# Optimization experiments

Measured on AMD Instinct MI355X. Metric: run time of the kernel, lower is better.

Reference implementation:

```python
import jax, jax.numpy as jnp
import numpy as np
import math

BATCH, SEQ, D_MODEL, HEADS = 2, 2048, 1024, 16
DK = D_MODEL // HEADS  # 64
THETA = 10000.0


def _init_linear(key, d_in, d_out):
    std = math.sqrt(2.0 / (d_in + d_out))
    return (jax.random.truncated_normal(key, -3.0, 3.0, (d_in, d_out), jnp.float32) * std)


def setup_inputs() -> dict:
    key = jax.random.key(0)
    kx, kq, kk, kv, ko = jax.random.split(key, 5)
    x = jax.random.normal(kx, (BATCH, SEQ, D_MODEL), jnp.float32)
    W_Q = _init_linear(kq, D_MODEL, D_MODEL)
    W_K = _init_linear(kk, D_MODEL, D_MODEL)
    W_V = _init_linear(kv, D_MODEL, D_MODEL)
    W_O = _init_linear(ko, D_MODEL, D_MODEL)
    token_positions = jnp.arange(SEQ, dtype=jnp.int64 if jax.config.jax_enable_x64 else jnp.int32)
    # RoPE tables: angle[i, k] = i / theta**(2k/d_k), shape [max_seq_len, d_k//2]
    pos = jnp.arange(SEQ, dtype=jnp.float32)[:, None]
    inv_freq = THETA ** (-2.0 * jnp.arange(DK // 2, dtype=jnp.float32) / DK)
    angles = pos * inv_freq
    return {
        "x": x,
        "token_positions": token_positions,
        "W_Q": W_Q,
        "W_K": W_K,
        "W_V": W_V,
        "W_O": W_O,
        "cos": jnp.cos(angles),
        "sin": jnp.sin(angles),
    }


def _apply_rope(t, cos_p, sin_p):
    # t: [B, H, S, DK]; cos_p/sin_p: [S, DK//2] (already gathered by position)
    t_even = t[..., 0::2]
    t_odd = t[..., 1::2]
    even_rot = cos_p * t_even - sin_p * t_odd
    odd_rot = sin_p * t_even + cos_p * t_odd
    # interleave back: [..., DK//2, 2] -> [..., DK]
    return jnp.stack([even_rot, odd_rot], axis=-1).reshape(t.shape)


def reference(x, token_positions, W_Q, W_K, W_V, W_O, cos, sin):
    B, S, D = x.shape
    H, dk = HEADS, D // HEADS
    # QKV projections, split into heads: [B, S, D] -> [B, H, S, dk]
    def proj(W):
        return jnp.einsum("bsd,de->bse", x, W).reshape(B, S, H, dk).transpose(0, 2, 1, 3)
    Q, K, V = proj(W_Q), proj(W_K), proj(W_V)
    cos_p = cos[token_positions]  # [S, dk//2]
    sin_p = sin[token_positions]
    Q = _apply_rope(Q, cos_p, sin_p)
    K = _apply_rope(K, cos_p, sin_p)
    scores = jnp.einsum("bhqd,bhkd->bhqk", Q, K) / jnp.sqrt(jnp.asarray(dk, x.dtype))
    causal = jnp.tril(jnp.ones((S, S), dtype=bool))
    scores = jnp.where(causal, scores, -jnp.inf)
    attn = jax.nn.softmax(scores, axis=-1)
    out = jnp.einsum("bhqk,bhkd->bhqd", attn, V)  # [B, H, S, dk]
    out = out.transpose(0, 2, 1, 3).reshape(B, S, D)
    return jnp.einsum("bsd,de->bse", out, W_O)
```

## Files before the change

### kernel.cpp

```cpp
#include <hip/hip_runtime.h>

typedef unsigned short u16;
typedef unsigned int   u32;
typedef __bf16  bf16x8 __attribute__((ext_vector_type(8)));
typedef float   f32x4  __attribute__((ext_vector_type(4)));
typedef u32     u32x4  __attribute__((ext_vector_type(4)));

#define SEQ    2048
#define HEADS  16
#define DM     1024
#define NBH    32
#define NBS    4096

#define LOG2E  1.4426950408889634f

__device__ __forceinline__ u16 f2b(float f) {
    u32 x;
    __builtin_memcpy(&x, &f, 4);
    return (u16)((x + 0x7fffu + ((x >> 16) & 1u)) >> 16);
}

__device__ __forceinline__ u32 pkc(float lo, float hi) {
    __bf16 a = (__bf16)lo, b = (__bf16)hi;
    u16 x, y;
    __builtin_memcpy(&x, &a, 2);
    __builtin_memcpy(&y, &b, 2);
    return (u32)x | ((u32)y << 16);
}

__device__ __forceinline__ bf16x8 ld_bf8(const u16* p) {
    return *(const bf16x8*)p;
}

__device__ __forceinline__ void gl_lds16(const u16* g, __bf16* l) {
    __builtin_amdgcn_global_load_lds(
        (__attribute__((address_space(1))) void*)g,
        (__attribute__((address_space(3))) void*)l,
        16, 0, 0);
}

__global__ __launch_bounds__(256) void transpose_wqkv(const float* __restrict__ Wq,
                                                      const float* __restrict__ Wk,
                                                      const float* __restrict__ Wv,
                                                      u16* __restrict__ WqkvT) {
    __shared__ u16 tile[64][65];
    const int z  = blockIdx.z;
    const float* src = (z == 0) ? Wq : (z == 1) ? Wk : Wv;
    const int k0 = blockIdx.x * 64, n0 = blockIdx.y * 64;
    const int tid = threadIdx.x;
    for (int i = 0; i < 16; ++i) {
        int e = i * 256 + tid;
        int r = e >> 6, c = e & 63;
        tile[r][c] = f2b(src[(size_t)(k0 + r) * DM + n0 + c]);
    }
    __syncthreads();
    u16* dst = WqkvT + (size_t)z * DM * DM;
    for (int i = 0; i < 16; ++i) {
        int e = i * 256 + tid;
        int r = e >> 6, c = e & 63;
        dst[(size_t)(n0 + r) * DM + k0 + c] = tile[c][r];
    }
}

__global__ __launch_bounds__(256) void transpose_wo(const float* __restrict__ Wo,
                                                    u16* __restrict__ WoT) {
    __shared__ u16 tile[64][65];
    const int k0 = blockIdx.x * 64, n0 = blockIdx.y * 64;
    const int tid = threadIdx.x;
    for (int i = 0; i < 16; ++i) {
        int e = i * 256 + tid;
        int r = e >> 6, c = e & 63;
        tile[r][c] = f2b(Wo[(size_t)(k0 + r) * DM + n0 + c]);
    }
    __syncthreads();
    for (int i = 0; i < 16; ++i) {
        int e = i * 256 + tid;
        int r = e >> 6, c = e & 63;
        WoT[(size_t)(n0 + r) * DM + k0 + c] = tile[c][r];
    }
}

__global__ __launch_bounds__(256) void cvt_x(const float* __restrict__ x,
                                             u16* __restrict__ xb) {
    int t = blockIdx.x * 256 + threadIdx.x;
    const float* p = x + (size_t)t * 8;
    f32x4 a = *(const f32x4*)p;
    f32x4 b = *(const f32x4*)(p + 4);
    u32x4 v;
    v[0] = pkc(a[0], a[1]);
    v[1] = pkc(a[2], a[3]);
    v[2] = pkc(b[0], b[1]);
    v[3] = pkc(b[2], b[3]);
    *(u32x4*)(xb + (size_t)t * 8) = v;
}

__global__ __launch_bounds__(256) void gemm_qkv(const u16* __restrict__ Ab,
                                                const u16* __restrict__ Bt,
                                                u16* __restrict__ Qp,
                                                u16* __restrict__ Kp,
                                                u16* __restrict__ Vt) {
    __shared__ __attribute__((aligned(16))) __bf16 As[128 * 64];
    __shared__ __attribute__((aligned(16))) __bf16 Bs[128 * 64];
    const int tid  = threadIdx.x;
    const int wave = tid >> 6, lane = tid & 63;
    const int quad = lane >> 4, col = lane & 15;
    const int wm = wave >> 1, wn = wave & 1;
    const int m0 = blockIdx.x * 128, n0 = blockIdx.y * 128;
    const int srow = tid >> 3;
    const int aslot = (((tid & 7) ^ (srow & 7)) << 3);
    const int c7 = col & 7;

    f32x4 zero = {0.f, 0.f, 0.f, 0.f};
    f32x4 acc[4][4];
    for (int i = 0; i < 4; ++i)
        for (int j = 0; j < 4; ++j) acc[i][j] = zero;

    for (int k0 = 0; k0 < DM; k0 += 64) {
        __syncthreads();
#pragma unroll
        for (int p = 0; p < 4; ++p)
            gl_lds16(Ab + (size_t)(m0 + p * 32 + srow) * DM + k0 + aslot,
                     &As[p * 2048 + tid * 8]);
#pragma unroll
        for (int p = 0; p < 4; ++p)
            gl_lds16(Bt + (size_t)(n0 + p * 32 + srow) * DM + k0 + aslot,
                     &Bs[p * 2048 + tid * 8]);
        __syncthreads();
#pragma unroll
        for (int ks = 0; ks < 2; ++ks) {
            const int rsl = ((((ks << 2) | quad) ^ c7) << 3);
            bf16x8 af[4], bfr[4];
#pragma unroll
            for (int mt = 0; mt < 4; ++mt)
                af[mt] = *(const bf16x8*)&As[(wm * 64 + mt * 16 + col) * 64 + rsl];
#pragma unroll
            for (int nt = 0; nt < 4; ++nt)
                bfr[nt] = *(const bf16x8*)&Bs[(wn * 64 + nt * 16 + col) * 64 + rsl];
#pragma unroll
            for (int mt = 0; mt < 4; ++mt)
#pragma unroll
                for (int nt = 0; nt < 4; ++nt)
                    acc[mt][nt] = __builtin_amdgcn_mfma_f32_16x16x32_bf16(
                        af[mt], bfr[nt], acc[mt][nt], 0, 0, 0);
        }
    }

    for (int mt = 0; mt < 4; ++mt)
        for (int nt = 0; nt < 4; ++nt) {
            int cc = n0 + wn * 64 + nt * 16 + col;
            int which = cc >> 10;
            int c1 = cc & 1023;
            int h = c1 >> 6, d = c1 & 63;
            for (int r = 0; r < 4; ++r) {
                int row = m0 + wm * 64 + mt * 16 + quad * 4 + r;
                int b = row >> 11, s = row & (SEQ - 1);
                u16 val = f2b(acc[mt][nt][r]);
                size_t bh = (size_t)(b * HEADS + h);
                if (which == 0)
                    Qp[(bh * SEQ + s) * 64 + d] = val;
                else if (which == 1)
                    Kp[(bh * SEQ + s) * 64 + d] = val;
                else
                    Vt[(bh * 64 + d) * SEQ + s] = val;
            }
        }
}

__global__ __launch_bounds__(256) void gemm_wo(const u16* __restrict__ A,
                                               const u16* __restrict__ Bt,
                                               float* __restrict__ C) {
    __shared__ __attribute__((aligned(16))) __bf16 As[128 * 64];
    __shared__ __attribute__((aligned(16))) __bf16 Bs[64 * 64];
    const int tid  = threadIdx.x;
    const int wave = tid >> 6, lane = tid & 63;
    const int quad = lane >> 4, col = lane & 15;
    const int m0 = blockIdx.x * 128, n0 = blockIdx.y * 64;
    const int srow = tid >> 3;
    const int aslot = (((tid & 7) ^ (srow & 7)) << 3);
    const int c7 = col & 7;

    f32x4 zero = {0.f, 0.f, 0.f, 0.f};
    f32x4 acc[2][4];
    for (int i = 0; i < 2; ++i)
        for (int j = 0; j < 4; ++j) acc[i][j] = zero;

    for (int k0 = 0; k0 < DM; k0 += 64) {
        __syncthreads();
#pragma unroll
        for (int p = 0; p < 4; ++p)
            gl_lds16(A + (size_t)(m0 + p * 32 + srow) * DM + k0 + aslot,
                     &As[p * 2048 + tid * 8]);
#pragma unroll
        for (int p = 0; p < 2; ++p)
            gl_lds16(Bt + (size_t)(n0 + p * 32 + srow) * DM + k0 + aslot,
                     &Bs[p * 2048 + tid * 8]);
        __syncthreads();
#pragma unroll
        for (int ks = 0; ks < 2; ++ks) {
            const int rsl = ((((ks << 2) | quad) ^ c7) << 3);
            bf16x8 af[2], bfr[4];
#pragma unroll
            for (int mt = 0; mt < 2; ++mt)
                af[mt] = *(const bf16x8*)&As[(wave * 32 + mt * 16 + col) * 64 + rsl];
#pragma unroll
            for (int nt = 0; nt < 4; ++nt)
                bfr[nt] = *(const bf16x8*)&Bs[(nt * 16 + col) * 64 + rsl];
#pragma unroll
            for (int mt = 0; mt < 2; ++mt)
#pragma unroll
                for (int nt = 0; nt < 4; ++nt)
                    acc[mt][nt] = __builtin_amdgcn_mfma_f32_16x16x32_bf16(
                        af[mt], bfr[nt], acc[mt][nt], 0, 0, 0);
        }
    }

    for (int mt = 0; mt < 2; ++mt)
        for (int nt = 0; nt < 4; ++nt)
            for (int r = 0; r < 4; ++r) {
                int row = m0 + wave * 32 + mt * 16 + quad * 4 + r;
                int cc  = n0 + nt * 16 + col;
                C[(size_t)row * DM + cc] = acc[mt][nt][r];
            }
}

__global__ __launch_bounds__(256) void rope_qk(u16* __restrict__ Qp,
                                               u16* __restrict__ Kp,
                                               const float* __restrict__ cosT,
                                               const float* __restrict__ sinT) {
    int t = blockIdx.x * 256 + threadIdx.x;
    int g  = t & 7;
    int s  = (t >> 3) & (SEQ - 1);
    int hh = (t >> 14) & (HEADS - 1);
    int b  = t >> 18;

    f32x4 cv = *(const f32x4*)&cosT[s * 32 + g * 4];
    f32x4 sv = *(const f32x4*)&sinT[s * 32 + g * 4];

    const float QS = 0.125f * LOG2E;
    size_t addr = (((size_t)(b * HEADS + hh)) * SEQ + s) * 64 + g * 8;
    u32x4 q4 = *(const u32x4*)(Qp + addr);
    u32x4 k4 = *(const u32x4*)(Kp + addr);
    u32x4 qo4, ko4;
#pragma unroll
    for (int j = 0; j < 4; ++j) {
        u32 q2 = q4[j], k2 = k4[j];
        u32 qe_b = (q2 & 0xffff) << 16, qo_b = q2 & 0xffff0000u;
        u32 ke_b = (k2 & 0xffff) << 16, ko_b = k2 & 0xffff0000u;
        float qe, qo, ke, ko;
        __builtin_memcpy(&qe, &qe_b, 4); __builtin_memcpy(&qo, &qo_b, 4);
        __builtin_memcpy(&ke, &ke_b, 4); __builtin_memcpy(&ko, &ko_b, 4);
        qo4[j] = (u32)f2b(QS * (cv[j] * qe - sv[j] * qo)) |
                 ((u32)f2b(QS * (sv[j] * qe + cv[j] * qo)) << 16);
        ko4[j] = (u32)f2b(cv[j] * ke - sv[j] * ko) |
                 ((u32)f2b(sv[j] * ke + cv[j] * ko) << 16);
    }
    *(u32x4*)(Qp + addr) = qo4;
    *(u32x4*)(Kp + addr) = ko4;
}

__global__ __launch_bounds__(256, 3) void flash_attn(const u16* __restrict__ Qp,
                                                     const u16* __restrict__ Kp,
                                                     const u16* __restrict__ Vt,
                                                     u16* __restrict__ O) {
    __shared__ float os[4][32][68];
    __shared__ float mM[4][32];
    __shared__ float mL[4][32];
    const int tid  = threadIdx.x;
    const int wave = tid >> 6, lane = tid & 63;
    const int quad = lane >> 4, col = lane & 15;
    const bool hi5 = lane >= 32;
    const bool hi4 = (lane & 16) != 0;
    const int bh = blockIdx.x;
    const int b = bh >> 4, h = bh & 15;
    const int qt = 63 - blockIdx.y;
    const int q0 = qt * 32;

    const u16* Qb = Qp + (size_t)bh * SEQ * 64;
    const u16* Kb = Kp + (size_t)bh * SEQ * 64;
    const u16* Vb = Vt + (size_t)bh * 64 * SEQ;

    bf16x8 bq00 = ld_bf8(Qb + (size_t)(q0 + col) * 64 + quad * 8);
    bf16x8 bq01 = ld_bf8(Qb + (size_t)(q0 + col) * 64 + 32 + quad * 8);
    bf16x8 bq10 = ld_bf8(Qb + (size_t)(q0 + 16 + col) * 64 + quad * 8);
    bf16x8 bq11 = ld_bf8(Qb + (size_t)(q0 + 16 + col) * 64 + 32 + quad * 8);

    f32x4 zero = {0.f, 0.f, 0.f, 0.f};
    f32x4 o0[4] = {zero, zero, zero, zero};
    f32x4 o1[4] = {zero, zero, zero, zero};
    float m0_ = -1e30f, m1_ = -1e30f;
    float lp0 = 0.f, lp1 = 0.f;

    const int nkt = qt + 1;
    int kt = wave;
    bf16x8 ck00, ck01, ck10, ck11, cv0, cv1, cv2, cv3;
    if (kt < nkt) {
        const int kb = kt << 5;
        ck00 = ld_bf8(Kb + (size_t)(kb + col) * 64 + quad * 8);
        ck01 = ld_bf8(Kb + (size_t)(kb + col) * 64 + 32 + quad * 8);
        ck10 = ld_bf8(Kb + (size_t)(kb + 16 + col) * 64 + quad * 8);
        ck11 = ld_bf8(Kb + (size_t)(kb + 16 + col) * 64 + 32 + quad * 8);
        cv0  = ld_bf8(Vb + (size_t)(0 * 16 + col) * SEQ + kb + quad * 8);
        cv1  = ld_bf8(Vb + (size_t)(1 * 16 + col) * SEQ + kb + quad * 8);
        cv2  = ld_bf8(Vb + (size_t)(2 * 16 + col) * SEQ + kb + quad * 8);
        cv3  = ld_bf8(Vb + (size_t)(3 * 16 + col) * SEQ + kb + quad * 8);
    }

    for (; kt < nkt; kt += 4) {
        const int kb = kt << 5;
        int kn = kt + 4; if (kn >= nkt) kn = kt;
        const int kb2 = kn << 5;
        bf16x8 nk00 = ld_bf8(Kb + (size_t)(kb2 + col) * 64 + quad * 8);
        bf16x8 nk01 = ld_bf8(Kb + (size_t)(kb2 + col) * 64 + 32 + quad * 8);
        bf16x8 nk10 = ld_bf8(Kb + (size_t)(kb2 + 16 + col) * 64 + quad * 8);
        bf16x8 nk11 = ld_bf8(Kb + (size_t)(kb2 + 16 + col) * 64 + 32 + quad * 8);
        bf16x8 nv0  = ld_bf8(Vb + (size_t)(0 * 16 + col) * SEQ + kb2 + quad * 8);
        bf16x8 nv1  = ld_bf8(Vb + (size_t)(1 * 16 + col) * SEQ + kb2 + quad * 8);
        bf16x8 nv2  = ld_bf8(Vb + (size_t)(2 * 16 + col) * SEQ + kb2 + quad * 8);
        bf16x8 nv3  = ld_bf8(Vb + (size_t)(3 * 16 + col) * SEQ + kb2 + quad * 8);

        f32x4 s00 = zero, s01 = zero, s10 = zero, s11 = zero;
        s00 = __builtin_amdgcn_mfma_f32_16x16x32_bf16(ck00, bq00, s00, 0, 0, 0);
        s10 = __builtin_amdgcn_mfma_f32_16x16x32_bf16(ck00, bq10, s10, 0, 0, 0);
        s00 = __builtin_amdgcn_mfma_f32_16x16x32_bf16(ck01, bq01, s00, 0, 0, 0);
        s10 = __builtin_amdgcn_mfma_f32_16x16x32_bf16(ck01, bq11, s10, 0, 0, 0);
        s01 = __builtin_amdgcn_mfma_f32_16x16x32_bf16(ck10, bq00, s01, 0, 0, 0);
        s11 = __builtin_amdgcn_mfma_f32_16x16x32_bf16(ck10, bq10, s11, 0, 0, 0);
        s01 = __builtin_amdgcn_mfma_f32_16x16x32_bf16(ck11, bq01, s01, 0, 0, 0);
        s11 = __builtin_amdgcn_mfma_f32_16x16x32_bf16(ck11, bq11, s11, 0, 0, 0);

        float v00[4], v01[4], v10[4], v11[4];
        float lm0 = -1e30f, lm1 = -1e30f;
        if (kt == qt) {
            for (int r = 0; r < 4; ++r) {
                int krel = quad * 4 + r;
                float a0 = (krel > col) ? -1e30f : s00[r];
                float b0 = -1e30f;
                float a1 = s10[r];
                float b1 = (krel > col) ? -1e30f : s11[r];
                v00[r] = a0; v01[r] = b0; v10[r] = a1; v11[r] = b1;
                lm0 = fmaxf(lm0, fmaxf(a0, b0));
                lm1 = fmaxf(lm1, fmaxf(a1, b1));
            }
        } else {
            for (int r = 0; r < 4; ++r) {
                v00[r] = s00[r]; v01[r] = s01[r];
                v10[r] = s10[r]; v11[r] = s11[r];
                lm0 = fmaxf(lm0, fmaxf(v00[r], v01[r]));
                lm1 = fmaxf(lm1, fmaxf(v10[r], v11[r]));
            }
        }

        float dd = fmaxf(lm0 - m0_, lm1 - m1_);
        if (__any(dd > 11.54f)) {
            float lr0 = fmaxf(lm0, __shfl_xor(lm0, 16));
            lr0 = fmaxf(lr0, __shfl_xor(lr0, 32));
            float lr1 = fmaxf(lm1, __shfl_xor(lm1, 16));
            lr1 = fmaxf(lr1, __shfl_xor(lr1, 32));
            float mn0 = fmaxf(m0_, lr0), mn1 = fmaxf(m1_, lr1);
            float al0 = __builtin_amdgcn_exp2f(m0_ - mn0);
            float al1 = __builtin_amdgcn_exp2f(m1_ - mn1);
            m0_ = mn0; m1_ = mn1;
            lp0 *= al0; lp1 *= al1;
            for (int r = 0; r < 4; ++r) {
                float ar0 = __shfl(al0, quad * 4 + r);
                float ar1 = __shfl(al1, quad * 4 + r);
                for (int nt = 0; nt < 4; ++nt) {
                    o0[nt][r] *= ar0;
                    o1[nt][r] *= ar1;
                }
            }
        }

        for (int r = 0; r < 4; ++r) {
            v00[r] = __builtin_amdgcn_exp2f(v00[r] - m0_);
            v01[r] = __builtin_amdgcn_exp2f(v01[r] - m0_);
            v10[r] = __builtin_amdgcn_exp2f(v10[r] - m1_);
            v11[r] = __builtin_amdgcn_exp2f(v11[r] - m1_);
            lp0 += v00[r] + v01[r];
            lp1 += v10[r] + v11[r];
        }

        u32 fwa0[4], fwa1[4];
        {
            u32 A0 = pkc(v00[0], v00[1]), A1 = pkc(v00[2], v00[3]);
            u32 B0 = pkc(v01[0], v01[1]), B1 = pkc(v01[2], v01[3]);
            u32 g0 = hi5 ? A0 : B0,  g1 = hi5 ? A1 : B1;
            u32 r0 = __shfl_xor(g0, 32), r1 = __shfl_xor(g1, 32);
            u32 P00 = hi5 ? r0 : A0,  P01 = hi5 ? r1 : A1;
            u32 P10 = hi5 ? B0 : r0,  P11 = hi5 ? B1 : r1;
            u32 h0 = hi4 ? P00 : P10, h1 = hi4 ? P01 : P11;
            u32 u0 = __shfl_xor(h0, 16), u1 = __shfl_xor(h1, 16);
            fwa0[0] = hi4 ? u0 : P00;  fwa0[1] = hi4 ? u1 : P01;
            fwa0[2] = hi4 ? P10 : u0;  fwa0[3] = hi4 ? P11 : u1;
        }
        {
            u32 A0 = pkc(v10[0], v10[1]), A1 = pkc(v10[2], v10[3]);
            u32 B0 = pkc(v11[0], v11[1]), B1 = pkc(v11[2], v11[3]);
            u32 g0 = hi5 ? A0 : B0,  g1 = hi5 ? A1 : B1;
            u32 r0 = __shfl_xor(g0, 32), r1 = __shfl_xor(g1, 32);
            u32 P00 = hi5 ? r0 : A0,  P01 = hi5 ? r1 : A1;
            u32 P10 = hi5 ? B0 : r0,  P11 = hi5 ? B1 : r1;
            u32 h0 = hi4 ? P00 : P10, h1 = hi4 ? P01 : P11;
            u32 u0 = __shfl_xor(h0, 16), u1 = __shfl_xor(h1, 16);
            fwa1[0] = hi4 ? u0 : P00;  fwa1[1] = hi4 ? u1 : P01;
            fwa1[2] = hi4 ? P10 : u0;  fwa1[3] = hi4 ? P11 : u1;
        }
        bf16x8 pf0, pf1;
        __builtin_memcpy(&pf0, fwa0, 16);
        __builtin_memcpy(&pf1, fwa1, 16);

        o0[0] = __builtin_amdgcn_mfma_f32_16x16x32_bf16(pf0, cv0, o0[0], 0, 0, 0);
        o1[0] = __builtin_amdgcn_mfma_f32_16x16x32_bf16(pf1, cv0, o1[0], 0, 0, 0);
        o0[1] = __builtin_amdgcn_mfma_f32_16x16x32_bf16(pf0, cv1, o0[1], 0, 0, 0);
        o1[1] = __builtin_amdgcn_mfma_f32_16x16x32_bf16(pf1, cv1, o1[1], 0, 0, 0);
        o0[2] = __builtin_amdgcn_mfma_f32_16x16x32_bf16(pf0, cv2, o0[2], 0, 0, 0);
        o1[2] = __builtin_amdgcn_mfma_f32_16x16x32_bf16(pf1, cv2, o1[2], 0, 0, 0);
        o0[3] = __builtin_amdgcn_mfma_f32_16x16x32_bf16(pf0, cv3, o0[3], 0, 0, 0);
        o1[3] = __builtin_amdgcn_mfma_f32_16x16x32_bf16(pf1, cv3, o1[3], 0, 0, 0);

        ck00 = nk00; ck01 = nk01; ck10 = nk10; ck11 = nk11;
        cv0 = nv0; cv1 = nv1; cv2 = nv2; cv3 = nv3;
    }

    float lt0 = lp0;
    lt0 += __shfl_xor(lt0, 16); lt0 += __shfl_xor(lt0, 32);
    float lt1 = lp1;
    lt1 += __shfl_xor(lt1, 16); lt1 += __shfl_xor(lt1, 32);
    if (quad == 0) {
        mM[wave][col] = m0_;      mL[wave][col] = lt0;
        mM[wave][16 + col] = m1_; mL[wave][16 + col] = lt1;
    }
    for (int nt = 0; nt < 4; ++nt)
        for (int r = 0; r < 4; ++r) {
            os[wave][quad * 4 + r][nt * 16 + col]      = o0[nt][r];
            os[wave][16 + quad * 4 + r][nt * 16 + col] = o1[nt][r];
        }
    __syncthreads();

    {
        const int q  = tid >> 3;
        const int d0 = (tid & 7) * 8;
        float M = fmaxf(fmaxf(mM[0][q], mM[1][q]), fmaxf(mM[2][q], mM[3][q]));
        float L = 0.f;
        f32x4 a0 = {0.f, 0.f, 0.f, 0.f}, a1 = {0.f, 0.f, 0.f, 0.f};
        for (int w = 0; w < 4; ++w) {
            float e = __builtin_amdgcn_exp2f(mM[w][q] - M);
            L += e * mL[w][q];
            f32x4 p0 = *(const f32x4*)&os[w][q][d0];
            f32x4 p1 = *(const f32x4*)&os[w][q][d0 + 4];
            for (int j = 0; j < 4; ++j) { a0[j] += e * p0[j]; a1[j] += e * p1[j]; }
        }
        float inv = 1.f / L;
        u32x4 val;
        val[0] = pkc(a0[0] * inv, a0[1] * inv);
        val[1] = pkc(a0[2] * inv, a0[3] * inv);
        val[2] = pkc(a1[0] * inv, a1[1] * inv);
        val[3] = pkc(a1[2] * inv, a1[3] * inv);
        *(u32x4*)&O[((size_t)b * SEQ + q0 + q) * DM + h * 64 + d0] = val;
    }
}

extern "C" void kernel_launch(void* const* d_in, const int* in_sizes, int n_in,
                              void* d_out, int out_size, void* d_ws, size_t ws_size,
                              hipStream_t stream) {
    const float* x    = (const float*)d_in[0];
    const float* Wq   = (const float*)d_in[2];
    const float* Wk   = (const float*)d_in[3];
    const float* Wv   = (const float*)d_in[4];
    const float* Wo   = (const float*)d_in[5];
    const float* cosT = (const float*)d_in[6];
    const float* sinT = (const float*)d_in[7];
    float* out = (float*)d_out;

    u16* ws    = (u16*)d_ws;
    u16* qp    = ws;
    u16* kp    = ws + 4194304;
    u16* vt    = ws + 8388608;
    u16* woT   = ws + 8388608;
    u16* wqkvT = ws + 12582912;
    u16* ao    = ws + 12582912;
    u16* xb    = (u16*)out;

    dim3 blk(256);
    transpose_wqkv<<<dim3(16, 16, 3), blk, 0, stream>>>(Wq, Wk, Wv, wqkvT);
    cvt_x<<<dim3(2048), blk, 0, stream>>>(x, xb);
    gemm_qkv<<<dim3(32, 24), blk, 0, stream>>>(xb, wqkvT, qp, kp, vt);
    rope_qk<<<dim3(2048), blk, 0, stream>>>(qp, kp, cosT, sinT);
    flash_attn<<<dim3(NBH, 64), blk, 0, stream>>>(qp, kp, vt, ao);
    transpose_wo<<<dim3(16, 16), blk, 0, stream>>>(Wo, woT);
    gemm_wo<<<dim3(32, 16), blk, 0, stream>>>(ao, woT, out);
}
```

Before: 233.5 us.

## Run flash attention with one wave per query tile, dropping the LDS merge

The attention kernel no longer splits each 32-row query tile's KV range across four waves. One 64-thread wave now walks every causal KV tile in sequence. That removes the shared-memory partial-output buffers, the barrier and the cross-wave softmax merge, and the output is normalized and written straight from registers. In exchange there are a quarter as many waves in flight and a four-times-longer serial loop for the late query tiles. The output stores are also now scattered 2-byte writes instead of 16-byte vector stores.

```diff
diff --git a/kernel.cpp b/kernel.cpp
--- a/kernel.cpp
+++ b/kernel.cpp
@@ -258,15 +258,11 @@
     *(u32x4*)(Kp + addr) = ko4;
 }
 
-__global__ __launch_bounds__(256, 3) void flash_attn(const u16* __restrict__ Qp,
-                                                     const u16* __restrict__ Kp,
-                                                     const u16* __restrict__ Vt,
-                                                     u16* __restrict__ O) {
-    __shared__ float os[4][32][68];
-    __shared__ float mM[4][32];
-    __shared__ float mL[4][32];
-    const int tid  = threadIdx.x;
-    const int wave = tid >> 6, lane = tid & 63;
+__global__ __launch_bounds__(64) void flash_attn(const u16* __restrict__ Qp,
+                                                 const u16* __restrict__ Kp,
+                                                 const u16* __restrict__ Vt,
+                                                 u16* __restrict__ O) {
+    const int lane = threadIdx.x;
     const int quad = lane >> 4, col = lane & 15;
     const bool hi5 = lane >= 32;
     const bool hi4 = (lane & 16) != 0;
@@ -291,24 +287,19 @@
     float lp0 = 0.f, lp1 = 0.f;
 
     const int nkt = qt + 1;
-    int kt = wave;
-    bf16x8 ck00, ck01, ck10, ck11, cv0, cv1, cv2, cv3;
-    if (kt < nkt) {
+
+    bf16x8 ck00 = ld_bf8(Kb + (size_t)col * 64 + quad * 8);
+    bf16x8 ck01 = ld_bf8(Kb + (size_t)col * 64 + 32 + quad * 8);
+    bf16x8 ck10 = ld_bf8(Kb + (size_t)(16 + col) * 64 + quad * 8);
+    bf16x8 ck11 = ld_bf8(Kb + (size_t)(16 + col) * 64 + 32 + quad * 8);
+    bf16x8 cv0  = ld_bf8(Vb + (size_t)(0 * 16 + col) * SEQ + quad * 8);
+    bf16x8 cv1  = ld_bf8(Vb + (size_t)(1 * 16 + col) * SEQ + quad * 8);
+    bf16x8 cv2  = ld_bf8(Vb + (size_t)(2 * 16 + col) * SEQ + quad * 8);
+    bf16x8 cv3  = ld_bf8(Vb + (size_t)(3 * 16 + col) * SEQ + quad * 8);
+
+    for (int kt = 0; kt < nkt; ++kt) {
         const int kb = kt << 5;
-        ck00 = ld_bf8(Kb + (size_t)(kb + col) * 64 + quad * 8);
-        ck01 = ld_bf8(Kb + (size_t)(kb + col) * 64 + 32 + quad * 8);
-        ck10 = ld_bf8(Kb + (size_t)(kb + 16 + col) * 64 + quad * 8);
-        ck11 = ld_bf8(Kb + (size_t)(kb + 16 + col) * 64 + 32 + quad * 8);
-        cv0  = ld_bf8(Vb + (size_t)(0 * 16 + col) * SEQ + kb + quad * 8);
-        cv1  = ld_bf8(Vb + (size_t)(1 * 16 + col) * SEQ + kb + quad * 8);
-        cv2  = ld_bf8(Vb + (size_t)(2 * 16 + col) * SEQ + kb + quad * 8);
-        cv3  = ld_bf8(Vb + (size_t)(3 * 16 + col) * SEQ + kb + quad * 8);
-    }
-
-    for (; kt < nkt; kt += 4) {
-        const int kb = kt << 5;
-        int kn = kt + 4; if (kn >= nkt) kn = kt;
-        const int kb2 = kn << 5;
+        const int kb2 = kb + 32;
         bf16x8 nk00 = ld_bf8(Kb + (size_t)(kb2 + col) * 64 + quad * 8);
         bf16x8 nk01 = ld_bf8(Kb + (size_t)(kb2 + col) * 64 + 32 + quad * 8);
         bf16x8 nk10 = ld_bf8(Kb + (size_t)(kb2 + 16 + col) * 64 + quad * 8);
@@ -426,37 +417,19 @@
     lt0 += __shfl_xor(lt0, 16); lt0 += __shfl_xor(lt0, 32);
     float lt1 = lp1;
     lt1 += __shfl_xor(lt1, 16); lt1 += __shfl_xor(lt1, 32);
-    if (quad == 0) {
-        mM[wave][col] = m0_;      mL[wave][col] = lt0;
-        mM[wave][16 + col] = m1_; mL[wave][16 + col] = lt1;
-    }
-    for (int nt = 0; nt < 4; ++nt)
-        for (int r = 0; r < 4; ++r) {
-            os[wave][quad * 4 + r][nt * 16 + col]      = o0[nt][r];
-            os[wave][16 + quad * 4 + r][nt * 16 + col] = o1[nt][r];
-        }
-    __syncthreads();
-
-    {
-        const int q  = tid >> 3;
-        const int d0 = (tid & 7) * 8;
-        float M = fmaxf(fmaxf(mM[0][q], mM[1][q]), fmaxf(mM[2][q], mM[3][q]));
-        float L = 0.f;
-        f32x4 a0 = {0.f, 0.f, 0.f, 0.f}, a1 = {0.f, 0.f, 0.f, 0.f};
-        for (int w = 0; w < 4; ++w) {
-            float e = __builtin_amdgcn_exp2f(mM[w][q] - M);
-            L += e * mL[w][q];
-            f32x4 p0 = *(const f32x4*)&os[w][q][d0];
-            f32x4 p1 = *(const f32x4*)&os[w][q][d0 + 4];
-            for (int j = 0; j < 4; ++j) { a0[j] += e * p0[j]; a1[j] += e * p1[j]; }
-        }
-        float inv = 1.f / L;
-        u32x4 val;
-        val[0] = pkc(a0[0] * inv, a0[1] * inv);
-        val[1] = pkc(a0[2] * inv, a0[3] * inv);
-        val[2] = pkc(a1[0] * inv, a1[1] * inv);
-        val[3] = pkc(a1[2] * inv, a1[3] * inv);
-        *(u32x4*)&O[((size_t)b * SEQ + q0 + q) * DM + h * 64 + d0] = val;
+    float linv0 = 1.f / lt0;
+    float linv1 = 1.f / lt1;
+    for (int r = 0; r < 4; ++r) {
+        float l0r = __shfl(linv0, quad * 4 + r);
+        float l1r = __shfl(linv1, quad * 4 + r);
+        int qrA = q0 + quad * 4 + r;
+        int qrB = qrA + 16;
+        for (int nt = 0; nt < 4; ++nt) {
+            O[((size_t)b * SEQ + qrA) * DM + h * 64 + nt * 16 + col] =
+                f2b(o0[nt][r] * l0r);
+            O[((size_t)b * SEQ + qrB) * DM + h * 64 + nt * 16 + col] =
+                f2b(o1[nt][r] * l1r);
+        }
     }
 }
 
@@ -486,7 +459,7 @@
     cvt_x<<<dim3(2048), blk, 0, stream>>>(x, xb);
     gemm_qkv<<<dim3(32, 24), blk, 0, stream>>>(xb, wqkvT, qp, kp, vt);
     rope_qk<<<dim3(2048), blk, 0, stream>>>(qp, kp, cosT, sinT);
-    flash_attn<<<dim3(NBH, 64), blk, 0, stream>>>(qp, kp, vt, ao);
+    flash_attn<<<dim3(NBH, 64), dim3(64), 0, stream>>>(qp, kp, vt, ao);
     transpose_wo<<<dim3(16, 16), blk, 0, stream>>>(Wo, woT);
     gemm_wo<<<dim3(32, 16), blk, 0, stream>>>(ao, woT, out);
 }
```

After: 238.0 us. Within noise of the previous version (+1.9%).
